# Performance work log

Hardware: AMD Instinct MI355X
Metric: run time of the kernel (lower is better)

Reference implementation:

```python
import jax, jax.numpy as jnp
import numpy as np

TAU = 0.5

def setup_inputs() -> dict:
    key = jax.random.key(0)
    ks = jax.random.split(key, 6)
    B, L, D, P = 4, 4096, 256, 256
    return {
        "X1": jax.random.normal(ks[0], (B, L, D), dtype=jnp.float32),
        "X2": jax.random.normal(ks[1], (B, L, D), dtype=jnp.float32),
        "W1": jax.random.normal(ks[2], (P, D), dtype=jnp.float32) * (1.0 / np.sqrt(D)),
        "b1": jax.random.normal(ks[3], (P,), dtype=jnp.float32) * 0.01,
        "W2": jax.random.normal(ks[4], (D, P), dtype=jnp.float32) * (1.0 / np.sqrt(P)),
        "b2": jax.random.normal(ks[5], (D,), dtype=jnp.float32) * 0.01,
    }

def _projection(z, W1, b1, W2, b2):
    h = jax.nn.elu(z @ W1.T + b1)
    return h @ W2.T + b2

def _normalize(z, eps=1e-12):
    n = jnp.linalg.norm(z, axis=-1, keepdims=True)
    return z / jnp.maximum(n, eps)

def _semi_loss(z1, z2, tau):
    # z1, z2: [B, L, D]
    z1n = _normalize(z1)
    z2n = _normalize(z2)
    refl = jnp.exp(jnp.einsum('bld,bmd->blm', z1n, z1n) / tau)   # [B, L, L]
    between = jnp.exp(jnp.einsum('bld,bmd->blm', z1n, z2n) / tau)
    refl_diag = jnp.diagonal(refl, axis1=-2, axis2=-1)           # [B, L]
    between_diag = jnp.diagonal(between, axis1=-2, axis2=-1)
    denom = refl.sum(axis=-1) + between.sum(axis=-1) - refl_diag
    return -jnp.log(between_diag / denom).sum(axis=-1)           # [B]

def reference(X1, X2, W1, b1, W2, b2):
    h1 = _projection(X1, W1, b1, W2, b2)
    h2 = _projection(X2, W1, b1, W2, b2)
    l1 = _semi_loss(h1, h2, TAU)
    l2 = _semi_loss(h2, h1, TAU)
    return ((l1 + l2) * 0.5).mean()
```

## Files before the change

### kernel.cpp

```cpp
#include <hip/hip_runtime.h>
#include <math.h>


typedef __attribute__((ext_vector_type(8))) short short8;
typedef __attribute__((ext_vector_type(4))) short short4v;
typedef __attribute__((ext_vector_type(4))) float float4v;
typedef __attribute__((ext_vector_type(8))) int int8v;
typedef __attribute__((ext_vector_type(4))) int int4v;

#if defined(__has_builtin)
#if __has_builtin(__builtin_amdgcn_exp2f)
#define EXP2F(x) __builtin_amdgcn_exp2f(x)
#endif
#endif
#ifndef EXP2F
#define EXP2F(x) __expf(0.69314718056f * (x))
#endif

__device__ __forceinline__ short f2bf(float f) {
    unsigned u = __builtin_bit_cast(unsigned, f);
    u += 0x7fffu + ((u >> 16) & 1u);
    return (short)(u >> 16);
}

__device__ __forceinline__ unsigned char f2fp8(float f) {
    float af = fabsf(f);
    unsigned s = (__builtin_bit_cast(unsigned, f) >> 31) << 7;
    if (af < 0.015625f) {
        int q = (int)rintf(af * 512.0f);
        return (unsigned char)(s | (unsigned)q);
    }
    unsigned au = __builtin_bit_cast(unsigned, af);
    au += 0x7FFFFu + ((au >> 20) & 1u);
    int e = (int)(au >> 23) - 127;
    unsigned m = (au >> 20) & 7u;
    return (unsigned char)(s | (unsigned)((e + 7) << 3) | m);
}

__device__ __forceinline__ void gl_lds16(const void* g, void* l) {
    __builtin_amdgcn_global_load_lds(
        (const __attribute__((address_space(1))) void*)g,
        (__attribute__((address_space(3))) void*)l, 16, 0, 0);
}

__device__ __forceinline__ void gemm256_core(
    const short* __restrict__ A, const short* __restrict__ B,
    int arow0, short* lsA, short* lsB, float4v acc[4][4])
{
    const int tid  = threadIdx.x;
    const int w    = tid >> 6;
    const int lane = tid & 63;
    const int l15  = lane & 15;

    for (int kt = 0; kt < 4; ++kt) {
        const int kbase = kt * 64;
#pragma unroll
        for (int r = 0; r < 10; ++r) {
            const int c = w * 10 + r;
            if (c < 8) {
                const int s   = c * 64 + lane;
                const int kc  = s >> 6;
                const int row = s & 63;
                gl_lds16(A + (size_t)(arow0 + row) * 256 + kbase + kc * 8,
                         lsA + (size_t)c * 512);
            } else {
                const int s   = (c - 8) * 64 + lane;
                const int kc  = s >> 8;
                const int row = s & 255;
                gl_lds16(B + (size_t)row * 256 + kbase + kc * 8,
                         lsB + (size_t)(c - 8) * 512);
            }
        }
        __syncthreads();
#pragma unroll
        for (int ks = 0; ks < 2; ++ks) {
            const int kc = ks * 4 + (lane >> 4);
            short8 af[4], bfv[4];
#pragma unroll
            for (int mi = 0; mi < 4; ++mi)
                af[mi] = *(const short8*)(lsA + ((size_t)kc * 64 + mi * 16 + l15) * 8);
#pragma unroll
            for (int ni = 0; ni < 4; ++ni)
                bfv[ni] = *(const short8*)(lsB + ((size_t)kc * 256 + w * 64 + ni * 16 + l15) * 8);
#pragma unroll
            for (int mi = 0; mi < 4; ++mi)
#pragma unroll
                for (int ni = 0; ni < 4; ++ni)
                    acc[mi][ni] = __builtin_amdgcn_mfma_f32_16x16x32_bf16(
                        af[mi], bfv[ni], acc[mi][ni], 0, 0, 0);
        }
        __syncthreads();
    }
}

__global__ __launch_bounds__(256) void convX_kernel(
    const float* __restrict__ X1, const float* __restrict__ X2,
    short* __restrict__ dst)
{
    int i = blockIdx.x * 256 + threadIdx.x;
    const float* src = (i < 1048576) ? X1 : X2;
    int j = i & 1048575;
    float4v v = ((const float4v*)src)[j];
    short4v o;
    o.x = f2bf(v.x); o.y = f2bf(v.y); o.z = f2bf(v.z); o.w = f2bf(v.w);
    ((short4v*)dst)[i] = o;
}

__global__ __launch_bounds__(256) void convW_kernel(
    const float* __restrict__ W1, const float* __restrict__ W2,
    short* __restrict__ d1, short* __restrict__ d2)
{
    int i = blockIdx.x * 256 + threadIdx.x;
    const float* src = (i < 16384) ? W1 : W2;
    short* dst = (i < 16384) ? d1 : d2;
    int j = i & 16383;
    float4v v = ((const float4v*)src)[j];
    short4v o;
    o.x = f2bf(v.x); o.y = f2bf(v.y); o.z = f2bf(v.z); o.w = f2bf(v.w);
    ((short4v*)dst)[j] = o;
}

__global__ __launch_bounds__(256, 4) void proj1_kernel(
    const short* __restrict__ Xbf, const short* __restrict__ W1bf,
    const float* __restrict__ b1, short* __restrict__ Hbf)
{
    __shared__ short lsA[4096];
    __shared__ short lsB[16384];
    const int arow0 = blockIdx.x * 64;
    float4v acc[4][4];
#pragma unroll
    for (int mi = 0; mi < 4; ++mi)
#pragma unroll
        for (int ni = 0; ni < 4; ++ni)
            acc[mi][ni] = (float4v){0.f, 0.f, 0.f, 0.f};

    gemm256_core(Xbf, W1bf, arow0, lsA, lsB, acc);

    const int tid  = threadIdx.x;
    const int w    = tid >> 6;
    const int lane = tid & 63;
    const int rowbase = arow0 + (lane >> 4) * 4;
    const int colbase = w * 64 + (lane & 15);
#pragma unroll
    for (int ni = 0; ni < 4; ++ni) {
        const int col = colbase + ni * 16;
        const float bv = b1[col];
#pragma unroll
        for (int mi = 0; mi < 4; ++mi)
#pragma unroll
            for (int reg = 0; reg < 4; ++reg) {
                const int row = rowbase + mi * 16 + reg;
                float v = acc[mi][ni][reg] + bv;
                v = (v > 0.f) ? v : expm1f(v);
                Hbf[(size_t)row * 256 + col] = f2bf(v);
            }
    }
}

__global__ __launch_bounds__(256, 4) void proj2norm_kernel(
    const short* __restrict__ Hbf, const short* __restrict__ W2bf,
    const float* __restrict__ b2, unsigned char* __restrict__ zn8)
{
    __shared__ short lsA[4096];
    __shared__ short lsB[16384];
    __shared__ float rssq[4][64];
    __shared__ float rinv[64];
    const int arow0 = blockIdx.x * 64;
    float4v acc[4][4];
#pragma unroll
    for (int mi = 0; mi < 4; ++mi)
#pragma unroll
        for (int ni = 0; ni < 4; ++ni)
            acc[mi][ni] = (float4v){0.f, 0.f, 0.f, 0.f};

    gemm256_core(Hbf, W2bf, arow0, lsA, lsB, acc);

    const int tid  = threadIdx.x;
    const int w    = tid >> 6;
    const int lane = tid & 63;
    const int quad = lane >> 4;
    const int l15  = lane & 15;

#pragma unroll
    for (int ni = 0; ni < 4; ++ni) {
        const float bv = b2[w * 64 + ni * 16 + l15];
#pragma unroll
        for (int mi = 0; mi < 4; ++mi)
#pragma unroll
            for (int reg = 0; reg < 4; ++reg)
                acc[mi][ni][reg] += bv;
    }
    float ps[4][4];
#pragma unroll
    for (int mi = 0; mi < 4; ++mi)
#pragma unroll
        for (int reg = 0; reg < 4; ++reg) {
            float s = 0.f;
#pragma unroll
            for (int ni = 0; ni < 4; ++ni) {
                float v = acc[mi][ni][reg];
                s += v * v;
            }
            s += __shfl_xor(s, 1); s += __shfl_xor(s, 2);
            s += __shfl_xor(s, 4); s += __shfl_xor(s, 8);
            ps[mi][reg] = s;
        }
    if (l15 == 0) {
#pragma unroll
        for (int mi = 0; mi < 4; ++mi)
#pragma unroll
            for (int reg = 0; reg < 4; ++reg)
                rssq[w][mi * 16 + quad * 4 + reg] = ps[mi][reg];
    }
    __syncthreads();
    if (tid < 64) {
        float ssq = rssq[0][tid] + rssq[1][tid] + rssq[2][tid] + rssq[3][tid];
        rinv[tid] = 1.69864360f / fmaxf(sqrtf(ssq), 1e-12f);
    }
    __syncthreads();

    const int r0  = arow0;
    const int set = r0 >> 14;
    const int bb  = (r0 >> 12) & 3;
    const int l0  = r0 & 4095;
    unsigned char* dst = zn8 + ((size_t)(bb * 2 + set) * 4096 + l0) * 256;
    const int colbase = w * 64 + l15;
#pragma unroll
    for (int mi = 0; mi < 4; ++mi)
#pragma unroll
        for (int reg = 0; reg < 4; ++reg) {
            const int rl = mi * 16 + quad * 4 + reg;
            const float inv = rinv[rl];
#pragma unroll
            for (int ni = 0; ni < 4; ++ni)
                dst[(size_t)rl * 256 + colbase + ni * 16] =
                    f2fp8(acc[mi][ni][reg] * inv);
        }
}

#if defined(__has_builtin)
#if __has_builtin(__builtin_amdgcn_mfma_scale_f32_16x16x128_f8f6f4)
#define HAVE_MX 1
#endif
#endif

__global__ __launch_bounds__(256, 2) void gram_fp8_sym_kernel(
    const unsigned char* __restrict__ zn8, float* __restrict__ S,
    float* __restrict__ Cc, float* __restrict__ out)
{
    __shared__ unsigned char lsB[2][32768];
    __shared__ float ldscol[128];

    const int bx    = blockIdx.x;
    const int xcd   = bx & 7;
    const int batch = xcd >> 1;
    const int sub   = (bx >> 3) * 2 + (xcd & 1);
    const int p     = sub >> 2;
    const int qu    = sub & 3;
    const int u0    = (qu == 0) ? 0 : 17 + (qu - 1) * 16;
    const int u1    = u0 + ((qu == 0) ? 17 : 16);
    const int ubrk  = 64 - p;

    const unsigned char* Z = zn8 + (size_t)batch * 2097152;

    const int tid  = threadIdx.x;
    const int w    = tid >> 6;
    const int lane = tid & 63;
    const int wm   = w & 1;
    const int wn   = w >> 1;
    const int quad = lane >> 4;
    const int l15  = lane & 15;

#define TJ_OF(u)  ((u) < ubrk ? p + (u) : (u) - 1)
#define ROW_OF(u) ((u) < ubrk ? p : 63 - p)

#define STAGE_B(t, buf)                                                       \
    {                                                                         \
        const unsigned char* Bb = Z + (size_t)(t) * 128 * 256;                \
        _Pragma("unroll")                                                     \
        for (int r = 0; r < 8; ++r) {                                         \
            const int c   = w * 8 + r;                                        \
            const int u_  = c * 64 + lane;                                    \
            const int kp  = u_ >> 7;                                          \
            const int col = u_ & 127;                                         \
            gl_lds16(Bb + (size_t)col * 256 + kp * 16,                        \
                     &lsB[buf][(size_t)c * 1024]);                            \
        }                                                                     \
    }

    float rs[4][4];
#pragma unroll
    for (int mi = 0; mi < 4; ++mi)
#pragma unroll
        for (int reg = 0; reg < 4; ++reg)
            rs[mi][reg] = 0.f;
    float dsum = 0.f;

#define FLUSH_RS(rowstripe)                                                   \
    {                                                                         \
        float* Sr = S + (size_t)batch * 8192 + (rowstripe) * 128 + wm * 64;   \
        _Pragma("unroll")                                                     \
        for (int mi = 0; mi < 4; ++mi)                                        \
            _Pragma("unroll")                                                 \
            for (int reg = 0; reg < 4; ++reg) {                               \
                float v = rs[mi][reg];                                        \
                v += __shfl_xor(v, 1); v += __shfl_xor(v, 2);                 \
                v += __shfl_xor(v, 4); v += __shfl_xor(v, 8);                 \
                if (l15 == 0)                                                 \
                    atomicAdd(&Sr[mi * 16 + quad * 4 + reg], v);              \
                rs[mi][reg] = 0.f;                                            \
            }                                                                 \
    }

    int currow = ROW_OF(u0);

#ifdef HAVE_MX
    int8v afr[4][2];
#define LOAD_A(rowstripe)                                                     \
    {                                                                         \
        const unsigned char* Ab = Z + (size_t)((rowstripe) * 128 + wm * 64) * 256; \
        _Pragma("unroll")                                                     \
        for (int mi = 0; mi < 4; ++mi)                                        \
            _Pragma("unroll")                                                 \
            for (int ks = 0; ks < 2; ++ks) {                                  \
                const unsigned char* pA = Ab + (size_t)(mi * 16 + l15) * 256  \
                                          + ks * 128 + quad * 32;             \
                int4v lo = *(const int4v*)pA;                                 \
                int4v hi = *(const int4v*)(pA + 16);                          \
                afr[mi][ks] = __builtin_shufflevector(lo, hi, 0,1,2,3,4,5,6,7); \
            }                                                                 \
    }
#else
    long afr[4][8];
#define LOAD_A(rowstripe)                                                     \
    {                                                                         \
        const unsigned char* Ab = Z + (size_t)((rowstripe) * 128 + wm * 64) * 256; \
        _Pragma("unroll")                                                     \
        for (int mi = 0; mi < 4; ++mi)                                        \
            _Pragma("unroll")                                                 \
            for (int kc = 0; kc < 8; ++kc)                                    \
                afr[mi][kc] = *(const long*)(Ab + (size_t)(mi * 16 + l15) * 256 \
                                             + kc * 32 + quad * 8);           \
    }
#endif

    LOAD_A(currow);
    STAGE_B(TJ_OF(u0), 0);
    __syncthreads();

    for (int ui = u0; ui < u1; ++ui) {
        const int buf = (ui - u0) & 1;
        const int row = ROW_OF(ui);
        const int tj  = TJ_OF(ui);
        if (row != currow) {
            FLUSH_RS(currow);
            LOAD_A(row);
            currow = row;
        }
        if (ui + 1 < u1) STAGE_B(TJ_OF(ui + 1), buf ^ 1);

        float4v acc[4][4];
#pragma unroll
        for (int mi = 0; mi < 4; ++mi)
#pragma unroll
            for (int ni = 0; ni < 4; ++ni)
                acc[mi][ni] = (float4v){0.f, 0.f, 0.f, 0.f};

        const unsigned char* lb = &lsB[buf][0];
#ifdef HAVE_MX
#pragma unroll
        for (int ks = 0; ks < 2; ++ks) {
            const int kp0 = ks * 8 + quad * 2;
            int8v bfv[4];
#pragma unroll
            for (int ni = 0; ni < 4; ++ni) {
                const unsigned char* pB = lb +
                    ((size_t)kp0 * 128 + wn * 64 + ni * 16 + l15) * 16;
                int4v lo = *(const int4v*)pB;
                int4v hi = *(const int4v*)(pB + 2048);
                bfv[ni] = __builtin_shufflevector(lo, hi, 0,1,2,3,4,5,6,7);
            }
#pragma unroll
            for (int mi = 0; mi < 4; ++mi)
#pragma unroll
                for (int ni = 0; ni < 4; ++ni)
                    acc[mi][ni] = __builtin_amdgcn_mfma_scale_f32_16x16x128_f8f6f4(
                        afr[mi][ks], bfv[ni], acc[mi][ni],
                        0, 0,
                        0, 0x7F7F7F7F,
                        0, 0x7F7F7F7F);
        }
#else
#pragma unroll
        for (int kc = 0; kc < 8; ++kc) {
            const int kseg = kc * 4 + quad;
            const int kp   = kseg >> 1;
            const int hf   = kseg & 1;
            long bfv[4];
#pragma unroll
            for (int ni = 0; ni < 4; ++ni)
                bfv[ni] = *(const long*)(lb +
                    ((size_t)kp * 128 + wn * 64 + ni * 16 + l15) * 16 + hf * 8);
#pragma unroll
            for (int mi = 0; mi < 4; ++mi)
#pragma unroll
                for (int ni = 0; ni < 4; ++ni)
                    acc[mi][ni] = __builtin_amdgcn_mfma_f32_16x16x32_fp8_fp8(
                        afr[mi][kc], bfv[ni], acc[mi][ni], 0, 0, 0);
        }
#endif

        if (tj == row + 32) {
#pragma unroll
            for (int mi = 0; mi < 4; ++mi)
#pragma unroll
                for (int ni = 0; ni < 4; ++ni)
#pragma unroll
                    for (int reg = 0; reg < 4; ++reg) {
                        const int r = wm * 64 + mi * 16 + quad * 4 + reg;
                        const int c = wn * 64 + ni * 16 + l15;
                        if (r == c) dsum += acc[mi][ni][reg];
                    }
        }

#pragma unroll
        for (int mi = 0; mi < 4; ++mi)
#pragma unroll
            for (int ni = 0; ni < 4; ++ni)
#pragma unroll
                for (int reg = 0; reg < 4; ++reg)
                    acc[mi][ni][reg] = EXP2F(acc[mi][ni][reg]);

#pragma unroll
        for (int mi = 0; mi < 4; ++mi)
#pragma unroll
            for (int reg = 0; reg < 4; ++reg)
                rs[mi][reg] += acc[mi][0][reg] + acc[mi][1][reg]
                             + acc[mi][2][reg] + acc[mi][3][reg];

        if (tj > row) {
            float cs[4];
#pragma unroll
            for (int ni = 0; ni < 4; ++ni) {
                float s = 0.f;
#pragma unroll
                for (int mi = 0; mi < 4; ++mi)
#pragma unroll
                    for (int reg = 0; reg < 4; ++reg)
                        s += acc[mi][ni][reg];
                s += __shfl_xor(s, 16); s += __shfl_xor(s, 32);
                cs[ni] = s;
            }
            if (wm == 0 && quad == 0) {
#pragma unroll
                for (int ni = 0; ni < 4; ++ni)
                    ldscol[wn * 64 + ni * 16 + l15] = cs[ni];
            }
            __syncthreads();
            if (wm == 1 && quad == 0) {
                float* Cd = Cc + ((size_t)batch * 64 + row) * 8192
                            + tj * 128 + wn * 64;
#pragma unroll
                for (int ni = 0; ni < 4; ++ni)
                    Cd[ni * 16 + l15] = cs[ni] + ldscol[wn * 64 + ni * 16 + l15];
            }
        }
        __syncthreads();
    }

    FLUSH_RS(currow);

    {
        float dv = dsum;
        dv += __shfl_xor(dv, 1);  dv += __shfl_xor(dv, 2);
        dv += __shfl_xor(dv, 4);  dv += __shfl_xor(dv, 8);
        dv += __shfl_xor(dv, 16); dv += __shfl_xor(dv, 32);
        if (lane == 0 && dv != 0.f)
            atomicAdd(out, -0.17328680f * dv);
    }
#undef STAGE_B
#undef LOAD_A
#undef FLUSH_RS
#undef TJ_OF
#undef ROW_OF
}

__global__ __launch_bounds__(256) void final_log_kernel(
    const float* __restrict__ S, const float* __restrict__ Cc,
    float* __restrict__ out)
{
    __shared__ float red[4];
    const int tid  = threadIdx.x;
    const int w    = tid >> 6;
    const int lane = tid & 63;
    const float E2 = 7.3890560989306495f;

    const int i = blockIdx.x * 256 + tid;
    const int b = i >> 13;
    const int q = i & 8191;
    float s = S[i];
    const float* Cp = Cc + (size_t)b * 64 * 8192 + q;
#pragma unroll 8
    for (int ti = 0; ti < 64; ++ti)
        s += Cp[(size_t)ti * 8192];
    float acc = logf(s - E2);

    acc += __shfl_xor(acc, 1);  acc += __shfl_xor(acc, 2);
    acc += __shfl_xor(acc, 4);  acc += __shfl_xor(acc, 8);
    acc += __shfl_xor(acc, 16); acc += __shfl_xor(acc, 32);
    if (lane == 0) red[w] = acc;
    __syncthreads();
    if (tid == 0)
        atomicAdd(out, 0.125f * (red[0] + red[1] + red[2] + red[3]));
}

extern "C" void kernel_launch(void* const* d_in, const int* in_sizes, int n_in,
                              void* d_out, int out_size, void* d_ws, size_t ws_size,
                              hipStream_t stream)
{
    const float* X1 = (const float*)d_in[0];
    const float* X2 = (const float*)d_in[1];
    const float* W1 = (const float*)d_in[2];
    const float* b1 = (const float*)d_in[3];
    const float* W2 = (const float*)d_in[4];
    const float* b2 = (const float*)d_in[5];

    char* ws = (char*)d_ws;
    float* S    = (float*)(ws + 0);
    short* W1bf = (short*)(ws + 131072);
    short* W2bf = (short*)(ws + 262144);
    short* Xbf  = (short*)(ws + 393216);
    unsigned char* zn8 = (unsigned char*)(ws + 393216);
    float* Cc   = (float*)(ws + 8781824);
    short* Hbf  = (short*)(ws + 17170432);

    hipMemsetAsync(S, 0, 131072, stream);
    hipMemsetAsync(d_out, 0, sizeof(float), stream);

    convW_kernel<<<128, 256, 0, stream>>>(W1, W2, W1bf, W2bf);
    convX_kernel<<<8192, 256, 0, stream>>>(X1, X2, Xbf);
    proj1_kernel<<<512, 256, 0, stream>>>(Xbf, W1bf, b1, Hbf);
    hipMemsetAsync(Cc, 0, 8388608, stream);
    proj2norm_kernel<<<512, 256, 0, stream>>>(Hbf, W2bf, b2, zn8);
    gram_fp8_sym_kernel<<<512, 256, 0, stream>>>(zn8, S, Cc, (float*)d_out);
    final_log_kernel<<<128, 256, 0, stream>>>(S, Cc, (float*)d_out);
}
```

Before: 214.8 us.

## Fuse projection GEMMs via LDS, drop Cc memset, raise MFMA priority

The two projection kernels become one kernel. The ELU hidden activations are written to LDS in a k-chunked layout and consumed directly by the second GEMM, so the bf16 hidden tensor no longer goes through global memory. The gram kernel now writes per-wave-half column partial sums to separate rows, which removes an LDS exchange and a barrier. The final kernel sums only the rows that were written, so the Cc memset can be dropped. s_setprio is also wrapped around the MFMA loop, and the fused kernel's occupancy hint falls from 4 to 2 blocks because of the larger LDS footprint.

```diff
diff --git a/kernel.cpp b/kernel.cpp
--- a/kernel.cpp
+++ b/kernel.cpp
@@ -120,66 +120,91 @@
     ((short4v*)dst)[j] = o;
 }
 
-__global__ __launch_bounds__(256, 4) void proj1_kernel(
+__global__ __launch_bounds__(256, 2) void fusedproj_kernel(
     const short* __restrict__ Xbf, const short* __restrict__ W1bf,
-    const float* __restrict__ b1, short* __restrict__ Hbf)
+    const float* __restrict__ b1, const short* __restrict__ W2bf,
+    const float* __restrict__ b2, unsigned char* __restrict__ zn8)
 {
     __shared__ short lsA[4096];
     __shared__ short lsB[16384];
-    const int arow0 = blockIdx.x * 64;
-    float4v acc[4][4];
-#pragma unroll
-    for (int mi = 0; mi < 4; ++mi)
-#pragma unroll
-        for (int ni = 0; ni < 4; ++ni)
-            acc[mi][ni] = (float4v){0.f, 0.f, 0.f, 0.f};
-
-    gemm256_core(Xbf, W1bf, arow0, lsA, lsB, acc);
-
-    const int tid  = threadIdx.x;
-    const int w    = tid >> 6;
-    const int lane = tid & 63;
-    const int rowbase = arow0 + (lane >> 4) * 4;
-    const int colbase = w * 64 + (lane & 15);
-#pragma unroll
-    for (int ni = 0; ni < 4; ++ni) {
-        const int col = colbase + ni * 16;
-        const float bv = b1[col];
-#pragma unroll
-        for (int mi = 0; mi < 4; ++mi)
-#pragma unroll
-            for (int reg = 0; reg < 4; ++reg) {
-                const int row = rowbase + mi * 16 + reg;
-                float v = acc[mi][ni][reg] + bv;
-                v = (v > 0.f) ? v : expm1f(v);
-                Hbf[(size_t)row * 256 + col] = f2bf(v);
-            }
-    }
-}
-
-__global__ __launch_bounds__(256, 4) void proj2norm_kernel(
-    const short* __restrict__ Hbf, const short* __restrict__ W2bf,
-    const float* __restrict__ b2, unsigned char* __restrict__ zn8)
-{
-    __shared__ short lsA[4096];
-    __shared__ short lsB[16384];
+    __shared__ short lsH[16384];
     __shared__ float rssq[4][64];
     __shared__ float rinv[64];
+
     const int arow0 = blockIdx.x * 64;
-    float4v acc[4][4];
-#pragma unroll
-    for (int mi = 0; mi < 4; ++mi)
-#pragma unroll
-        for (int ni = 0; ni < 4; ++ni)
-            acc[mi][ni] = (float4v){0.f, 0.f, 0.f, 0.f};
-
-    gemm256_core(Hbf, W2bf, arow0, lsA, lsB, acc);
-
     const int tid  = threadIdx.x;
     const int w    = tid >> 6;
     const int lane = tid & 63;
     const int quad = lane >> 4;
     const int l15  = lane & 15;
+
+    float4v acc[4][4];
+#pragma unroll
+    for (int mi = 0; mi < 4; ++mi)
+#pragma unroll
+        for (int ni = 0; ni < 4; ++ni)
+            acc[mi][ni] = (float4v){0.f, 0.f, 0.f, 0.f};
+
+    gemm256_core(Xbf, W1bf, arow0, lsA, lsB, acc);
+
+    {
+        const int rowbase = quad * 4;
+        const int colbase = w * 64 + l15;
+#pragma unroll
+        for (int ni = 0; ni < 4; ++ni) {
+            const int p  = colbase + ni * 16;
+            const float bv = b1[p];
+#pragma unroll
+            for (int mi = 0; mi < 4; ++mi)
+#pragma unroll
+                for (int reg = 0; reg < 4; ++reg) {
+                    const int row = rowbase + mi * 16 + reg;
+                    float v = acc[mi][ni][reg] + bv;
+                    v = (v > 0.f) ? v : expm1f(v);
+                    lsH[(size_t)(p >> 3) * 512 + row * 8 + (p & 7)] = f2bf(v);
+                }
+        }
+    }
+
+#pragma unroll
+    for (int mi = 0; mi < 4; ++mi)
+#pragma unroll
+        for (int ni = 0; ni < 4; ++ni)
+            acc[mi][ni] = (float4v){0.f, 0.f, 0.f, 0.f};
+
+    for (int kt = 0; kt < 4; ++kt) {
+        const int kbase = kt * 64;
+#pragma unroll
+        for (int r = 0; r < 8; ++r) {
+            const int c   = w * 8 + r;
+            const int s   = c * 64 + lane;
+            const int kc  = s >> 8;
+            const int row = s & 255;
+            gl_lds16(W2bf + (size_t)row * 256 + kbase + kc * 8,
+                     lsB + (size_t)c * 512);
+        }
+        __syncthreads();
+#pragma unroll
+        for (int ks = 0; ks < 2; ++ks) {
+            const int kc = ks * 4 + quad;
+            short8 af[4], bfv[4];
+#pragma unroll
+            for (int mi = 0; mi < 4; ++mi)
+                af[mi] = *(const short8*)(lsH +
+                    ((size_t)(kt * 8 + kc) * 64 + mi * 16 + l15) * 8);
+#pragma unroll
+            for (int ni = 0; ni < 4; ++ni)
+                bfv[ni] = *(const short8*)(lsB +
+                    ((size_t)kc * 256 + w * 64 + ni * 16 + l15) * 8);
+#pragma unroll
+            for (int mi = 0; mi < 4; ++mi)
+#pragma unroll
+                for (int ni = 0; ni < 4; ++ni)
+                    acc[mi][ni] = __builtin_amdgcn_mfma_f32_16x16x32_bf16(
+                        af[mi], bfv[ni], acc[mi][ni], 0, 0, 0);
+        }
+        __syncthreads();
+    }
 
 #pragma unroll
     for (int ni = 0; ni < 4; ++ni) {
@@ -249,7 +274,6 @@
     float* __restrict__ Cc, float* __restrict__ out)
 {
     __shared__ unsigned char lsB[2][32768];
-    __shared__ float ldscol[128];
 
     const int bx    = blockIdx.x;
     const int xcd   = bx & 7;
@@ -367,6 +391,7 @@
                 acc[mi][ni] = (float4v){0.f, 0.f, 0.f, 0.f};
 
         const unsigned char* lb = &lsB[buf][0];
+        __builtin_amdgcn_s_setprio(1);
 #ifdef HAVE_MX
 #pragma unroll
         for (int ks = 0; ks < 2; ++ks) {
@@ -409,6 +434,7 @@
                         afr[mi][kc], bfv[ni], acc[mi][ni], 0, 0, 0);
         }
 #endif
+        __builtin_amdgcn_s_setprio(0);
 
         if (tj == row + 32) {
 #pragma unroll
@@ -439,7 +465,8 @@
                              + acc[mi][2][reg] + acc[mi][3][reg];
 
         if (tj > row) {
-            float cs[4];
+            float* Cd = Cc + ((size_t)batch * 128 + row * 2 + wm) * 8192
+                        + tj * 128 + wn * 64;
 #pragma unroll
             for (int ni = 0; ni < 4; ++ni) {
                 float s = 0.f;
@@ -449,20 +476,8 @@
                     for (int reg = 0; reg < 4; ++reg)
                         s += acc[mi][ni][reg];
                 s += __shfl_xor(s, 16); s += __shfl_xor(s, 32);
-                cs[ni] = s;
-            }
-            if (wm == 0 && quad == 0) {
-#pragma unroll
-                for (int ni = 0; ni < 4; ++ni)
-                    ldscol[wn * 64 + ni * 16 + l15] = cs[ni];
-            }
-            __syncthreads();
-            if (wm == 1 && quad == 0) {
-                float* Cd = Cc + ((size_t)batch * 64 + row) * 8192
-                            + tj * 128 + wn * 64;
-#pragma unroll
-                for (int ni = 0; ni < 4; ++ni)
-                    Cd[ni * 16 + l15] = cs[ni] + ldscol[wn * 64 + ni * 16 + l15];
+                if (quad == 0)
+                    Cd[ni * 16 + l15] = s;
             }
         }
         __syncthreads();
@@ -499,10 +514,10 @@
     const int b = i >> 13;
     const int q = i & 8191;
     float s = S[i];
-    const float* Cp = Cc + (size_t)b * 64 * 8192 + q;
-#pragma unroll 8
-    for (int ti = 0; ti < 64; ++ti)
-        s += Cp[(size_t)ti * 8192];
+    const float* Cp = Cc + (size_t)b * 128 * 8192 + q;
+    const int np = (q >> 7) * 2;
+    for (int r = 0; r < np; ++r)
+        s += Cp[(size_t)r * 8192];
     float acc = logf(s - E2);
 
     acc += __shfl_xor(acc, 1);  acc += __shfl_xor(acc, 2);
@@ -530,18 +545,15 @@
     short* W1bf = (short*)(ws + 131072);
     short* W2bf = (short*)(ws + 262144);
     short* Xbf  = (short*)(ws + 393216);
-    unsigned char* zn8 = (unsigned char*)(ws + 393216);
-    float* Cc   = (float*)(ws + 8781824);
-    short* Hbf  = (short*)(ws + 17170432);
+    float* Cc   = (float*)(ws + 393216);
+    unsigned char* zn8 = (unsigned char*)(ws + 17170432);
 
     hipMemsetAsync(S, 0, 131072, stream);
     hipMemsetAsync(d_out, 0, sizeof(float), stream);
 
     convW_kernel<<<128, 256, 0, stream>>>(W1, W2, W1bf, W2bf);
     convX_kernel<<<8192, 256, 0, stream>>>(X1, X2, Xbf);
-    proj1_kernel<<<512, 256, 0, stream>>>(Xbf, W1bf, b1, Hbf);
-    hipMemsetAsync(Cc, 0, 8388608, stream);
-    proj2norm_kernel<<<512, 256, 0, stream>>>(Hbf, W2bf, b2, zn8);
+    fusedproj_kernel<<<512, 256, 0, stream>>>(Xbf, W1bf, b1, W2bf, b2, zn8);
     gram_fp8_sym_kernel<<<512, 256, 0, stream>>>(zn8, S, Cc, (float*)d_out);
     final_log_kernel<<<128, 256, 0, stream>>>(S, Cc, (float*)d_out);
 }
```

New measurement: 213.7 us. No clear change (-0.5%).
